# Kernel optimization log

Measured on AMD Instinct MI355X. Metric: run time of the kernel, lower is better.

## Reference

```python
import jax, jax.numpy as jnp
import numpy as np

D_MODEL = 1024
N_HEADS = 16
HEAD_DIM = D_MODEL // N_HEADS


def setup_inputs() -> dict:
    key = jax.random.key(0)
    k_x, k_w1, k_b1, k_w2, k_b2 = jax.random.split(key, 5)
    B, S = 4, 2048
    x = jax.random.normal(k_x, (B, S, D_MODEL), dtype=jnp.float32)
    # torch Linear init ~ U(-1/sqrt(fan_in), 1/sqrt(fan_in))
    lim = 1.0 / np.sqrt(D_MODEL)
    qkv_w = jax.random.uniform(k_w1, (D_MODEL, 3 * D_MODEL), jnp.float32, -lim, lim)
    qkv_b = jax.random.uniform(k_b1, (3 * D_MODEL,), jnp.float32, -lim, lim)
    out_w = jax.random.uniform(k_w2, (D_MODEL, D_MODEL), jnp.float32, -lim, lim)
    out_b = jax.random.uniform(k_b2, (D_MODEL,), jnp.float32, -lim, lim)
    return {"x": x, "qkv_w": qkv_w, "qkv_b": qkv_b, "out_w": out_w, "out_b": out_b}


def reference(x, qkv_w, qkv_b, out_w, out_b):
    B, S, D = x.shape
    scale = HEAD_DIM ** -0.5
    qkv = x @ qkv_w + qkv_b  # [B,S,3D]
    q, k, v = jnp.split(qkv, 3, axis=-1)
    def to_heads(t):
        return t.reshape(B, S, N_HEADS, HEAD_DIM).transpose(0, 2, 1, 3)  # [B,H,S,Dh]
    q, k, v = to_heads(q), to_heads(k), to_heads(v)
    scores = jnp.einsum('bhqd,bhkd->bhqk', q, k) * scale  # [B,H,S,S]
    causal = jnp.tril(jnp.ones((S, S), dtype=bool))
    scores = jnp.where(causal, scores, -jnp.inf)
    weights = jax.nn.softmax(scores, axis=-1)  # dropout is identity in eval
    out = jnp.einsum('bhqk,bhkd->bhqd', weights, v)  # [B,H,S,Dh]
    out = out.transpose(0, 2, 1, 3).reshape(B, S, D)
    return out @ out_w + out_b
```

## Files before the change

### kernel.cpp

```cpp
#include <hip/hip_runtime.h>

typedef __bf16 bf16x8 __attribute__((ext_vector_type(8)));
typedef float f32x4 __attribute__((ext_vector_type(4)));
typedef unsigned short u16;

#define D_MODEL 1024
#define SEQ     2048
#define BATCH   4
#define NH      16
#define DH      64

static __device__ __forceinline__ u16 f2bf(float f) {
    union { float f; unsigned u; } v; v.f = f;
    unsigned r = v.u + 0x7FFF + ((v.u >> 16) & 1);
    return (u16)(r >> 16);
}
static __device__ __forceinline__ void storeC(u16* C, size_t off, float v) { C[off] = f2bf(v); }
static __device__ __forceinline__ void storeC(float* C, size_t off, float v) { C[off] = v; }

static __device__ __forceinline__ void async_ld16(u16* lds, const u16* g) {
    __builtin_amdgcn_global_load_lds(
        (const __attribute__((address_space(1))) unsigned int*)g,
        (__attribute__((address_space(3))) unsigned int*)lds, 16, 0, 0);
}

__global__ __launch_bounds__(256) void cvt_bf16(const float* __restrict__ in,
                                                u16* __restrict__ out) {
    size_t i = ((size_t)blockIdx.x * 256 + threadIdx.x) * 8;
    float4 a = *(const float4*)(in + i);
    float4 b = *(const float4*)(in + i + 4);
    u16 t[8] = {f2bf(a.x), f2bf(a.y), f2bf(a.z), f2bf(a.w),
                f2bf(b.x), f2bf(b.y), f2bf(b.z), f2bf(b.w)};
    *(uint4*)(out + i) = *(uint4*)t;
}

__global__ void transpose_w(const float* __restrict__ in, u16* __restrict__ out,
                            int K, int N) {
    __shared__ float tile[32][33];
    int n0 = blockIdx.x * 32, k0 = blockIdx.y * 32;
    int tx = threadIdx.x, ty = threadIdx.y;
    for (int i = ty; i < 32; i += 8)
        tile[i][tx] = in[(size_t)(k0 + i) * N + n0 + tx];
    __syncthreads();
    for (int i = ty; i < 32; i += 8)
        out[(size_t)(n0 + i) * K + k0 + tx] = f2bf(tile[tx][i]);
}

template <typename CT>
__global__ __launch_bounds__(256) void gemm_bt(
    const u16* __restrict__ A, int lda,
    const u16* __restrict__ Bt, int ldb,
    const float* __restrict__ bias,
    CT* __restrict__ C, int ldc, int K) {
    __shared__ u16 As[128 * 64];
    __shared__ u16 Bs[128 * 64];
    int m0 = blockIdx.x * 128, n0 = blockIdx.y * 128;
    int tid = threadIdx.x;
    int w = tid >> 6, lane = tid & 63, l15 = lane & 15, g = lane >> 4;
    int wm = (w & 1) * 64, wn = (w >> 1) * 64;
    int srow = w * 8 + (lane >> 3);
    int sk8  = lane & 7;

    f32x4 acc[4][4] = {};
    for (int kt = 0; kt < K; kt += 64) {
        #pragma unroll
        for (int p = 0; p < 4; ++p) {
            int row = p * 32 + srow;
            int k8 = sk8 ^ (row & 7);
            async_ld16(&As[p * 2048 + w * 512],
                       A + (size_t)(m0 + row) * lda + kt + k8 * 8);
            async_ld16(&Bs[p * 2048 + w * 512],
                       Bt + (size_t)(n0 + row) * ldb + kt + k8 * 8);
        }
        __syncthreads();
        #pragma unroll
        for (int kk = 0; kk < 2; ++kk) {
            bf16x8 af[4], bf_[4];
            int s8 = ((kk << 2) | g) ^ (l15 & 7);
            #pragma unroll
            for (int i = 0; i < 4; ++i) {
                af[i]  = *(const bf16x8*)&As[(wm + i * 16 + l15) * 64 + s8 * 8];
                bf_[i] = *(const bf16x8*)&Bs[(wn + i * 16 + l15) * 64 + s8 * 8];
            }
            #pragma unroll
            for (int i = 0; i < 4; ++i)
                #pragma unroll
                for (int j = 0; j < 4; ++j)
                    acc[i][j] = __builtin_amdgcn_mfma_f32_16x16x32_bf16(
                        af[i], bf_[j], acc[i][j], 0, 0, 0);
        }
        __syncthreads();
    }
    #pragma unroll
    for (int j = 0; j < 4; ++j) {
        int n = n0 + wn + j * 16 + l15;
        float bv = bias[n];
        #pragma unroll
        for (int i = 0; i < 4; ++i) {
            int mbase = m0 + wm + i * 16 + g * 4;
            #pragma unroll
            for (int r = 0; r < 4; ++r)
                storeC(C, (size_t)(mbase + r) * ldc + n, acc[i][j][r] + bv);
        }
    }
}

__global__ __launch_bounds__(512, 2) void gemm_qkv(
    const u16* __restrict__ A,
    const u16* __restrict__ Bt,
    const float* __restrict__ bias,
    u16* __restrict__ Qd, u16* __restrict__ pkK, u16* __restrict__ pkV) {
    __shared__ u16 As[2][16384];
    __shared__ u16 Bs[2][16384];
    const int K = D_MODEL;

    int lid = blockIdx.x;
    int swz = (lid & 7) * 48 + (lid >> 3);
    int m0 = (swz & 31) * 256;
    int n0 = (swz >> 5) * 256;

    int tid = threadIdx.x;
    int w = tid >> 6, lane = tid & 63, l15 = lane & 15, g = lane >> 4;
    int wm = (w >> 2) * 128, wn = (w & 3) * 64;
    int srow = tid >> 3, sg = tid & 7;

    const u16* Ab = A + (size_t)m0 * K;
    const u16* Bb = Bt + (size_t)n0 * K;

    auto stageA = [&](int buf, int c, int kt) {
        int row = c * 64 + srow;
        int k8 = sg ^ (row & 7);
        async_ld16(&As[buf][(c * 64 + w * 8) * 64],
                   Ab + (size_t)row * K + kt + k8 * 8);
    };
    auto stageB = [&](int buf, int c, int kt) {
        int row = c * 64 + srow;
        int k8 = sg ^ (row & 7);
        async_ld16(&Bs[buf][(c * 64 + w * 8) * 64],
                   Bb + (size_t)row * K + kt + k8 * 8);
    };
    auto rdA = [&](int cur, int i, int kk) {
        return *(const bf16x8*)&As[cur][(wm + i * 16 + l15) * 64 +
                                        ((((kk << 2) | g) ^ (l15 & 7)) * 8)];
    };
    auto rdB = [&](int cur, int j, int kk) {
        return *(const bf16x8*)&Bs[cur][(wn + j * 16 + l15) * 64 +
                                        ((((kk << 2) | g) ^ (l15 & 7)) * 8)];
    };

    f32x4 acc[8][4] = {};

    stageB(0, 0, 0); stageB(0, 1, 0); stageB(0, 2, 0); stageB(0, 3, 0);
    stageA(0, 0, 0); stageA(0, 2, 0); stageA(0, 1, 0); stageA(0, 3, 0);
    asm volatile("s_waitcnt vmcnt(2)" ::: "memory");
    __builtin_amdgcn_s_barrier();

#define PHASE(i0, STAGE_STMT, ENDWAIT_STMT)                                      \
    do {                                                                         \
        bf16x8 a00 = rdA(cur, (i0), 0), a01 = rdA(cur, (i0), 1);                 \
        bf16x8 a10 = rdA(cur, (i0) + 1, 0), a11 = rdA(cur, (i0) + 1, 1);         \
        STAGE_STMT;                                                              \
        __builtin_amdgcn_s_barrier();                                            \
        asm volatile("s_waitcnt lgkmcnt(0)" ::: "memory");                       \
        __builtin_amdgcn_s_setprio(1);                                           \
        _Pragma("unroll")                                                        \
        for (int j = 0; j < 4; ++j) {                                            \
            acc[(i0)][j] = __builtin_amdgcn_mfma_f32_16x16x32_bf16(              \
                a00, bfr[j][0], acc[(i0)][j], 0, 0, 0);                          \
            acc[(i0)][j] = __builtin_amdgcn_mfma_f32_16x16x32_bf16(              \
                a01, bfr[j][1], acc[(i0)][j], 0, 0, 0);                          \
            acc[(i0) + 1][j] = __builtin_amdgcn_mfma_f32_16x16x32_bf16(          \
                a10, bfr[j][0], acc[(i0) + 1][j], 0, 0, 0);                      \
            acc[(i0) + 1][j] = __builtin_amdgcn_mfma_f32_16x16x32_bf16(          \
                a11, bfr[j][1], acc[(i0) + 1][j], 0, 0, 0);                      \
        }                                                                        \
        __builtin_amdgcn_s_setprio(0);                                           \
        ENDWAIT_STMT;                                                            \
        __builtin_amdgcn_s_barrier();                                            \
    } while (0)

    for (int kt = 0; kt < K; kt += 64) {
        int cur = (kt >> 6) & 1, nxt = cur ^ 1;
        int ktn = kt + 64;
        bool hn = ktn < K;

        bf16x8 bfr[4][2];
        #pragma unroll
        for (int j = 0; j < 4; ++j)
            #pragma unroll
            for (int kk = 0; kk < 2; ++kk)
                bfr[j][kk] = rdB(cur, j, kk);

        PHASE(0,
              if (hn) { stageB(nxt, 0, ktn); stageB(nxt, 1, ktn); },
              );
        PHASE(2,
              if (hn) { stageB(nxt, 2, ktn); stageB(nxt, 3, ktn); },
              if (hn) { asm volatile("s_waitcnt vmcnt(4)" ::: "memory"); }
              else    { asm volatile("s_waitcnt vmcnt(0)" ::: "memory"); });
        PHASE(4,
              if (hn) { stageA(nxt, 0, ktn); stageA(nxt, 2, ktn); },
              );
        PHASE(6,
              if (hn) { stageA(nxt, 1, ktn); stageA(nxt, 3, ktn); },
              asm volatile("s_waitcnt vmcnt(2)" ::: "memory"); );
    }
#undef PHASE

    #pragma unroll
    for (int j = 0; j < 4; ++j) {
        int n = n0 + wn + j * 16 + l15;
        float bv = bias[n];
        int region = n >> 10;
        int hd = n & 1023;
        int h = hd >> 6, d = hd & 63;
        #pragma unroll
        for (int i = 0; i < 8; ++i) {
            #pragma unroll
            for (int r = 0; r < 4; ++r) {
                int m = m0 + wm + i * 16 + g * 4 + r;
                u16 vb = f2bf(acc[i][j][r] + bv);
                int b = m >> 11, s = m & 2047;
                int t = s >> 6, kap = s & 63;
                if (region == 0) {
                    Qd[(size_t)m * 1024 + hd] = vb;
                } else if (region == 1) {
                    int bh = b * 16 + h;
                    int nb = kap >> 4, lk = kap & 15;
                    int kk = d >> 5, gk = (d >> 3) & 3, jk = d & 7;
                    pkK[(size_t)(bh * 32 + t) * 4096 +
                        ((nb * 2 + kk) * 64 + gk * 16 + lk) * 8 + jk] = vb;
                } else {
                    int bh = b * 16 + h;
                    int kk = kap >> 5, gv = (kap >> 3) & 3, jv = kap & 7;
                    int nb = d >> 4, lv = d & 15;
                    pkV[(size_t)(bh * 32 + t) * 4096 +
                        ((nb * 2 + kk) * 64 + gv * 16 + lv) * 8 + jv] = vb;
                }
            }
        }
    }
}

__global__ __launch_bounds__(256) void attn_flash(
    u16* __restrict__ Qd, const u16* __restrict__ pkK,
    const u16* __restrict__ pkV) {
    __shared__ __align__(16) char smemraw[18432 + 256];
    u16 (*Pt)[32][72] = (u16(*)[32][72])smemraw;
    float* Om = (float*)smemraw;
    float* Lm = (float*)(smemraw + 18432);

    int bh = blockIdx.x, b = bh >> 4, h = bh & 15;
    int tid = threadIdx.x;
    int w = tid >> 6, lane = tid & 63, l15 = lane & 15, g = lane >> 4;
    int wq = w >> 1, wk = w & 1;

    const u16* Kb = pkK + (size_t)bh * 32 * 4096;
    const u16* Vb = pkV + (size_t)bh * 32 * 4096;
    u16* Qbase = Qd + (size_t)b * SEQ * 1024 + h * DH;

    int qts[2] = {31 - (int)blockIdx.y, (int)blockIdx.y};

    #pragma unroll
    for (int qi = 0; qi < 2; ++qi) {
        int qt = qts[qi];
        int q0 = qt * 64;

        bf16x8 qfrag[2][2];
        #pragma unroll
        for (int st = 0; st < 2; ++st) {
            const u16* qp = Qbase + (size_t)(q0 + wq * 32 + st * 16 + l15) * 1024 + g * 8;
            bf16x8 a = *(const bf16x8*)qp;
            bf16x8 c = *(const bf16x8*)(qp + 32);
            #pragma unroll
            for (int jj = 0; jj < 8; ++jj) {
                a[jj] = (__bf16)((float)a[jj] * 0.125f);
                c[jj] = (__bf16)((float)c[jj] * 0.125f);
            }
            qfrag[st][0] = a; qfrag[st][1] = c;
        }

        f32x4 o[2][4] = {};
        float lsum[2][4] = {};

        for (int t = wk; t <= qt; t += 2) {
            const u16* kt = Kb + t * 4096;
            const u16* vt = Vb + t * 4096;
            bf16x8 kf[4][2], vf[4][2];
            #pragma unroll
            for (int nb = 0; nb < 4; ++nb) {
                #pragma unroll
                for (int kk = 0; kk < 2; ++kk) {
                    kf[nb][kk] = *(const bf16x8*)(kt + ((nb * 2 + kk) * 64 + lane) * 8);
                    vf[nb][kk] = *(const bf16x8*)(vt + ((nb * 2 + kk) * 64 + lane) * 8);
                }
            }
            bool diag = (t == qt);
            int k0 = t * 64;

            #pragma unroll
            for (int st = 0; st < 2; ++st) {
                f32x4 s[4] = {};
                #pragma unroll
                for (int nb = 0; nb < 4; ++nb)
                    #pragma unroll
                    for (int kk = 0; kk < 2; ++kk)
                        s[nb] = __builtin_amdgcn_mfma_f32_16x16x32_bf16(
                            qfrag[st][kk], kf[nb][kk], s[nb], 0, 0, 0);

                #pragma unroll
                for (int r = 0; r < 4; ++r) {
                    int qg = q0 + wq * 32 + st * 16 + g * 4 + r;
                    #pragma unroll
                    for (int nb = 0; nb < 4; ++nb) {
                        float p = __expf(s[nb][r]);
                        if (diag && (k0 + nb * 16 + l15) > qg) p = 0.f;
                        lsum[st][r] += p;
                        Pt[w][st * 16 + g * 4 + r][nb * 16 + l15] =
                            (u16)(__float_as_uint(p) >> 16);
                    }
                }

                #pragma unroll
                for (int kk = 0; kk < 2; ++kk) {
                    bf16x8 aP = *(const bf16x8*)&Pt[w][st * 16 + l15][kk * 32 + g * 8];
                    #pragma unroll
                    for (int nb = 0; nb < 4; ++nb)
                        o[st][nb] = __builtin_amdgcn_mfma_f32_16x16x32_bf16(
                            aP, vf[nb][kk], o[st][nb], 0, 0, 0);
                }
            }
        }

        #pragma unroll
        for (int msk = 1; msk < 16; msk <<= 1)
            #pragma unroll
            for (int st = 0; st < 2; ++st)
                #pragma unroll
                for (int r = 0; r < 4; ++r)
                    lsum[st][r] += __shfl_xor(lsum[st][r], msk, 64);

        __syncthreads();
        if (wk == 0) {
            #pragma unroll
            for (int st = 0; st < 2; ++st)
                #pragma unroll
                for (int r = 0; r < 4; ++r) {
                    int qrow = wq * 32 + st * 16 + g * 4 + r;
                    if (l15 == 0) Lm[qrow] = lsum[st][r];
                    #pragma unroll
                    for (int nb = 0; nb < 4; ++nb)
                        Om[qrow * 65 + nb * 16 + l15] = o[st][nb][r];
                }
        }
        __syncthreads();
        if (wk == 1) {
            #pragma unroll
            for (int st = 0; st < 2; ++st)
                #pragma unroll
                for (int r = 0; r < 4; ++r) {
                    int qrow = wq * 32 + st * 16 + g * 4 + r;
                    float inv = 1.f / (lsum[st][r] + Lm[qrow]);
                    u16* op = Qbase + (size_t)(q0 + qrow) * 1024;
                    #pragma unroll
                    for (int nb = 0; nb < 4; ++nb) {
                        float val = (o[st][nb][r] + Om[qrow * 65 + nb * 16 + l15]) * inv;
                        op[nb * 16 + l15] = f2bf(val);
                    }
                }
        }
        __syncthreads();
    }
}

extern "C" void kernel_launch(void* const* d_in, const int* in_sizes, int n_in,
                              void* d_out, int out_size, void* d_ws, size_t ws_size,
                              hipStream_t stream) {
    const float* x     = (const float*)d_in[0];
    const float* qkv_w = (const float*)d_in[1];
    const float* qkv_b = (const float*)d_in[2];
    const float* out_w = (const float*)d_in[3];
    const float* out_b = (const float*)d_in[4];
    float* out = (float*)d_out;

    const int M = BATCH * SEQ;
    u16* Qd     = (u16*)d_ws;
    u16* pkK    = Qd  + (size_t)M * D_MODEL;
    u16* pkV    = pkK + (size_t)64 * 32 * 4096;
    u16* xb     = pkV + (size_t)64 * 32 * 4096;
    u16* Wqkv_t = xb  + (size_t)M * D_MODEL;
    u16* Wout_t = Wqkv_t + (size_t)3 * D_MODEL * D_MODEL;

    cvt_bf16<<<(size_t)M * D_MODEL / (256 * 8), 256, 0, stream>>>(x, xb);
    transpose_w<<<dim3(3 * D_MODEL / 32, D_MODEL / 32), dim3(32, 8), 0, stream>>>(
        qkv_w, Wqkv_t, D_MODEL, 3 * D_MODEL);
    transpose_w<<<dim3(D_MODEL / 32, D_MODEL / 32), dim3(32, 8), 0, stream>>>(
        out_w, Wout_t, D_MODEL, D_MODEL);

    gemm_qkv<<<dim3(384), 512, 0, stream>>>(xb, Wqkv_t, qkv_b, Qd, pkK, pkV);

    attn_flash<<<dim3(BATCH * NH, SEQ / 64 / 2), 256, 0, stream>>>(Qd, pkK, pkV);

    gemm_bt<float><<<dim3(M / 128, D_MODEL / 128), 256, 0, stream>>>(
        Qd, D_MODEL, Wout_t, D_MODEL, out_b, out, D_MODEL, D_MODEL);
}
```

Measured before the change: 277.8 us.

## Retile QKV GEMM to 256x192, double-buffer output GEMM, prioritize attention MFMAs

The QKV projection GEMM moves from 256x256 tiles on 384 blocks to 256x192 tiles on 512 blocks. Blocks are mapped so each XCD handles a contiguous band of M rows, and the async load schedule is reworked for three B chunks. The output-projection GEMM gains a second LDS buffer so the next K tile is prefetched while the current one feeds the MFMAs. In the attention kernel, s_setprio is raised around the MFMA sections so matrix work gets issue priority over the softmax code. The aim is better CU fill, less load-latency stall and better overlap, at the cost of smaller per-block B reuse in QKV and twice the LDS in the output GEMM.

```diff
diff --git a/kernel.cpp b/kernel.cpp
--- a/kernel.cpp
+++ b/kernel.cpp
@@ -52,8 +52,8 @@
     const u16* __restrict__ Bt, int ldb,
     const float* __restrict__ bias,
     CT* __restrict__ C, int ldc, int K) {
-    __shared__ u16 As[128 * 64];
-    __shared__ u16 Bs[128 * 64];
+    __shared__ u16 As[2][128 * 64];
+    __shared__ u16 Bs[2][128 * 64];
     int m0 = blockIdx.x * 128, n0 = blockIdx.y * 128;
     int tid = threadIdx.x;
     int w = tid >> 6, lane = tid & 63, l15 = lane & 15, g = lane >> 4;
@@ -61,26 +61,33 @@
     int srow = w * 8 + (lane >> 3);
     int sk8  = lane & 7;
 
-    f32x4 acc[4][4] = {};
-    for (int kt = 0; kt < K; kt += 64) {
+    auto stage = [&](int buf, int kt) {
         #pragma unroll
         for (int p = 0; p < 4; ++p) {
             int row = p * 32 + srow;
             int k8 = sk8 ^ (row & 7);
-            async_ld16(&As[p * 2048 + w * 512],
+            async_ld16(&As[buf][p * 2048 + w * 512],
                        A + (size_t)(m0 + row) * lda + kt + k8 * 8);
-            async_ld16(&Bs[p * 2048 + w * 512],
+            async_ld16(&Bs[buf][p * 2048 + w * 512],
                        Bt + (size_t)(n0 + row) * ldb + kt + k8 * 8);
         }
-        __syncthreads();
+    };
+
+    f32x4 acc[4][4] = {};
+
+    stage(0, 0);
+    __syncthreads();
+    for (int kt = 0; kt < K; kt += 64) {
+        int cur = (kt >> 6) & 1;
+        if (kt + 64 < K) stage(cur ^ 1, kt + 64);
         #pragma unroll
         for (int kk = 0; kk < 2; ++kk) {
             bf16x8 af[4], bf_[4];
             int s8 = ((kk << 2) | g) ^ (l15 & 7);
             #pragma unroll
             for (int i = 0; i < 4; ++i) {
-                af[i]  = *(const bf16x8*)&As[(wm + i * 16 + l15) * 64 + s8 * 8];
-                bf_[i] = *(const bf16x8*)&Bs[(wn + i * 16 + l15) * 64 + s8 * 8];
+                af[i]  = *(const bf16x8*)&As[cur][(wm + i * 16 + l15) * 64 + s8 * 8];
+                bf_[i] = *(const bf16x8*)&Bs[cur][(wn + i * 16 + l15) * 64 + s8 * 8];
             }
             #pragma unroll
             for (int i = 0; i < 4; ++i)
@@ -110,18 +117,18 @@
     const u16* __restrict__ Bt,
     const float* __restrict__ bias,
     u16* __restrict__ Qd, u16* __restrict__ pkK, u16* __restrict__ pkV) {
-    __shared__ u16 As[2][16384];
-    __shared__ u16 Bs[2][16384];
+    __shared__ u16 As[2][256 * 64];
+    __shared__ u16 Bs[2][192 * 64];
     const int K = D_MODEL;
 
     int lid = blockIdx.x;
-    int swz = (lid & 7) * 48 + (lid >> 3);
-    int m0 = (swz & 31) * 256;
-    int n0 = (swz >> 5) * 256;
+    int xcd = lid & 7, p = lid >> 3;
+    int m0 = (xcd * 4 + (p >> 4)) * 256;
+    int n0 = (p & 15) * 192;
 
     int tid = threadIdx.x;
     int w = tid >> 6, lane = tid & 63, l15 = lane & 15, g = lane >> 4;
-    int wm = (w >> 2) * 128, wn = (w & 3) * 64;
+    int wm = (w >> 2) * 128, wn = (w & 3) * 48;
     int srow = tid >> 3, sg = tid & 7;
 
     const u16* Ab = A + (size_t)m0 * K;
@@ -148,9 +155,9 @@
                                         ((((kk << 2) | g) ^ (l15 & 7)) * 8)];
     };
 
-    f32x4 acc[8][4] = {};
-
-    stageB(0, 0, 0); stageB(0, 1, 0); stageB(0, 2, 0); stageB(0, 3, 0);
+    f32x4 acc[8][3] = {};
+
+    stageB(0, 0, 0); stageB(0, 1, 0); stageB(0, 2, 0);
     stageA(0, 0, 0); stageA(0, 2, 0); stageA(0, 1, 0); stageA(0, 3, 0);
     asm volatile("s_waitcnt vmcnt(2)" ::: "memory");
     __builtin_amdgcn_s_barrier();
@@ -164,7 +171,7 @@
         asm volatile("s_waitcnt lgkmcnt(0)" ::: "memory");                       \
         __builtin_amdgcn_s_setprio(1);                                           \
         _Pragma("unroll")                                                        \
-        for (int j = 0; j < 4; ++j) {                                            \
+        for (int j = 0; j < 3; ++j) {                                            \
             acc[(i0)][j] = __builtin_amdgcn_mfma_f32_16x16x32_bf16(              \
                 a00, bfr[j][0], acc[(i0)][j], 0, 0, 0);                          \
             acc[(i0)][j] = __builtin_amdgcn_mfma_f32_16x16x32_bf16(              \
@@ -184,9 +191,9 @@
         int ktn = kt + 64;
         bool hn = ktn < K;
 
-        bf16x8 bfr[4][2];
-        #pragma unroll
-        for (int j = 0; j < 4; ++j)
+        bf16x8 bfr[3][2];
+        #pragma unroll
+        for (int j = 0; j < 3; ++j)
             #pragma unroll
             for (int kk = 0; kk < 2; ++kk)
                 bfr[j][kk] = rdB(cur, j, kk);
@@ -195,20 +202,20 @@
               if (hn) { stageB(nxt, 0, ktn); stageB(nxt, 1, ktn); },
               );
         PHASE(2,
-              if (hn) { stageB(nxt, 2, ktn); stageB(nxt, 3, ktn); },
+              if (hn) { stageB(nxt, 2, ktn); stageA(nxt, 0, ktn); },
               if (hn) { asm volatile("s_waitcnt vmcnt(4)" ::: "memory"); }
               else    { asm volatile("s_waitcnt vmcnt(0)" ::: "memory"); });
         PHASE(4,
-              if (hn) { stageA(nxt, 0, ktn); stageA(nxt, 2, ktn); },
+              if (hn) { stageA(nxt, 2, ktn); stageA(nxt, 1, ktn); },
               );
         PHASE(6,
-              if (hn) { stageA(nxt, 1, ktn); stageA(nxt, 3, ktn); },
+              if (hn) { stageA(nxt, 3, ktn); },
               asm volatile("s_waitcnt vmcnt(2)" ::: "memory"); );
     }
 #undef PHASE
 
     #pragma unroll
-    for (int j = 0; j < 4; ++j) {
+    for (int j = 0; j < 3; ++j) {
         int n = n0 + wn + j * 16 + l15;
         float bv = bias[n];
         int region = n >> 10;
@@ -301,12 +308,14 @@
             #pragma unroll
             for (int st = 0; st < 2; ++st) {
                 f32x4 s[4] = {};
+                __builtin_amdgcn_s_setprio(1);
                 #pragma unroll
                 for (int nb = 0; nb < 4; ++nb)
                     #pragma unroll
                     for (int kk = 0; kk < 2; ++kk)
                         s[nb] = __builtin_amdgcn_mfma_f32_16x16x32_bf16(
                             qfrag[st][kk], kf[nb][kk], s[nb], 0, 0, 0);
+                __builtin_amdgcn_s_setprio(0);
 
                 #pragma unroll
                 for (int r = 0; r < 4; ++r) {
@@ -321,6 +330,7 @@
                     }
                 }
 
+                __builtin_amdgcn_s_setprio(1);
                 #pragma unroll
                 for (int kk = 0; kk < 2; ++kk) {
                     bf16x8 aP = *(const bf16x8*)&Pt[w][st * 16 + l15][kk * 32 + g * 8];
@@ -329,6 +339,7 @@
                         o[st][nb] = __builtin_amdgcn_mfma_f32_16x16x32_bf16(
                             aP, vf[nb][kk], o[st][nb], 0, 0, 0);
                 }
+                __builtin_amdgcn_s_setprio(0);
             }
         }
 
@@ -397,7 +408,7 @@
     transpose_w<<<dim3(D_MODEL / 32, D_MODEL / 32), dim3(32, 8), 0, stream>>>(
         out_w, Wout_t, D_MODEL, D_MODEL);
 
-    gemm_qkv<<<dim3(384), 512, 0, stream>>>(xb, Wqkv_t, qkv_b, Qd, pkK, pkV);
+    gemm_qkv<<<dim3(512), 512, 0, stream>>>(xb, Wqkv_t, qkv_b, Qd, pkK, pkV);
 
     attn_flash<<<dim3(BATCH * NH, SEQ / 64 / 2), 256, 0, stream>>>(Qd, pkK, pkV);
 
```

Measured after the change: 266.1 us. 1.04x faster.
